# Kernel tuning notes

Hardware: AMD Instinct MI355X
Metric: run time of the kernel (lower is better)

## Reference

```python
import jax, jax.numpy as jnp
import numpy as np
from jax import lax

IN_CH = 512
OUT_CH = 512
KERNEL = 3
STYLE_DIM = 512
BATCH = 8
HW = 64
EPS = 1e-08
LR_MUL = 1.0


def setup_inputs() -> dict:
    key = jax.random.key(0)
    k1, k2, k3, k4 = jax.random.split(key, 4)
    x = jax.random.normal(k1, (BATCH, IN_CH, HW, HW), dtype=jnp.float32)
    style = jax.random.normal(k2, (BATCH, STYLE_DIM), dtype=jnp.float32)
    weight = jax.random.normal(k3, (1, OUT_CH, IN_CH, KERNEL, KERNEL), dtype=jnp.float32)
    mod_weight = jax.random.normal(k4, (IN_CH, STYLE_DIM), dtype=jnp.float32)
    mod_bias = jnp.ones((IN_CH,), dtype=jnp.float32)  # bias_init=1
    return {"x": x, "style": style, "weight": weight,
            "mod_weight": mod_weight, "mod_bias": mod_bias}


def reference(x, style, weight, mod_weight, mod_bias):
    batch, in_ch, h, w_dim = x.shape
    conv_scale = 1.0 / np.sqrt(in_ch * KERNEL * KERNEL)
    lin_scale = 1.0 / np.sqrt(STYLE_DIM) * LR_MUL

    # EqualizedLinear modulation: style -> per-channel scale, shape (B, in_ch)
    s = style @ (mod_weight * lin_scale).T + mod_bias * LR_MUL

    # Modulate: (B, out, in, k, k)
    w = conv_scale * weight * s[:, None, :, None, None]
    # Demodulate
    demod = lax.rsqrt(jnp.sum(w * w, axis=(2, 3, 4)) + EPS)  # (B, out)
    w = w * demod[:, :, None, None, None]

    pad = KERNEL // 2

    def conv_one(xi, wi):
        # xi: (in, H, W), wi: (out, in, k, k)
        return lax.conv_general_dilated(
            xi[None], wi, window_strides=(1, 1),
            padding=[(pad, pad), (pad, pad)],
            dimension_numbers=("NCHW", "OIHW", "NCHW"))[0]

    out = jax.vmap(conv_one)(x, w)  # (B, out, H, W)
    return out
```

## Files before the change

kernel.cpp:

```cpp
#include <hip/hip_runtime.h>
#include <hip/hip_bf16.h>
#include <cstdint>

#define IN_CH 512
#define OUT_CH 512
#define STYLE_DIM 512
#define BATCH 8
#define HW 64

typedef __bf16 bf16x8 __attribute__((ext_vector_type(8)));
typedef float f32x16 __attribute__((ext_vector_type(16)));

__device__ __forceinline__ void gload_lds16(const void* g, void* l) {
  __builtin_amdgcn_global_load_lds(
      (const __attribute__((address_space(1))) unsigned int*)g,
      (__attribute__((address_space(3))) unsigned int*)l,
      16, 0, 0);
}

#define WAITV(N) asm volatile("s_waitcnt vmcnt(" #N ")" ::: "memory")
#define BARRIER() do { asm volatile("" ::: "memory"); __builtin_amdgcn_s_barrier(); \
                       asm volatile("" ::: "memory"); } while (0)

__global__ void k_prepA(const float* __restrict__ style, const float* __restrict__ modw,
                        const float* __restrict__ modb, const float* __restrict__ w,
                        float* __restrict__ s_out, float* __restrict__ wsq,
                        __bf16* __restrict__ wgp) {
  const int tid = threadIdx.x;
  if (blockIdx.x < 128) {
    __shared__ float st[BATCH * STYLE_DIM];
    for (int i = tid; i < BATCH * STYLE_DIM; i += 256) st[i] = style[i];
    __syncthreads();
    const int ic = blockIdx.x * 4 + (tid >> 6);
    const int l = tid & 63;
    const float* mr = modw + (size_t)ic * STYLE_DIM + l * 8;
    float m[8];
    #pragma unroll
    for (int j = 0; j < 8; ++j) m[j] = mr[j];
    float accs[8];
    #pragma unroll
    for (int b = 0; b < 8; ++b) {
      const float* sb = st + b * STYLE_DIM + l * 8;
      float a = 0.f;
      #pragma unroll
      for (int j = 0; j < 8; ++j) a += m[j] * sb[j];
      accs[b] = a;
    }
    #pragma unroll
    for (int off = 32; off; off >>= 1) {
      #pragma unroll
      for (int b = 0; b < 8; ++b) accs[b] += __shfl_down(accs[b], off, 64);
    }
    if (l == 0) {
      #pragma unroll
      for (int b = 0; b < 8; ++b)
        s_out[b * IN_CH + ic] = accs[b] * 0.04419417382415922f + modb[ic];
    }
  } else {
    const int idx = (blockIdx.x - 128) * 256 + tid;
    const int oc = idx >> 9, ic = idx & 511;
    const int octile = oc >> 8, R = oc & 255, j = R >> 1;
    const int chunk = ic >> 6, sslot = (ic >> 3) & 7, e = ic & 7;
    const int p = 2 * ((sslot + j) & 7) + (R & 1);
    const int u = j * 16 + p;
    const float* pw = w + ((size_t)oc * IN_CH + ic) * 9;
    float sum = 0.f;
    #pragma unroll
    for (int t = 0; t < 9; ++t) {
      float v = pw[t];
      sum += v * v;
      wgp[((size_t)((t * 8 + chunk) * 2 + octile) * 2048 + u) * 8 + e] = (__bf16)v;
    }
    wsq[oc * IN_CH + ic] = sum;
  }
}

__global__ void k_prepB(const float* __restrict__ x, const float* __restrict__ s,
                        const float* __restrict__ wsq,
                        __bf16* __restrict__ xgp, float* __restrict__ scale) {
  const int t = threadIdx.x;
  if (blockIdx.x < 512) {
    const int b = blockIdx.x >> 6, y = blockIdx.x & 63;
    const int xcol = t & 63;
    const int g0 = t >> 6;
    const float* sr = s + b * IN_CH;
    const size_t rowbase = ((size_t)(b * 64 + y)) * 8 * 528;
    #pragma unroll
    for (int i = 0; i < 8; ++i) {
      const int g = i * 8 + g0;
      bf16x8 pk;
      #pragma unroll
      for (int e = 0; e < 8; ++e) {
        const int ic = g * 8 + e;
        pk[e] = (__bf16)(x[(((size_t)(b * IN_CH) + ic) * HW + y) * HW + xcol] * sr[ic]);
      }
      const int col = xcol + 1, c = col >> 1;
      const int p = 2 * (((g & 7) + c) & 7) + (col & 1);
      const int u = c * 16 + p;
      *(bf16x8*)(xgp + (rowbase + (size_t)(g >> 3) * 528 + u) * 8) = pk;
    }
    if (t < 128) {
      const int col = (t & 1) * 65, g = t >> 1;
      const int c = col >> 1;
      const int p = 2 * (((g & 7) + c) & 7) + (col & 1);
      const int u = c * 16 + p;
      bf16x8 z = {};
      *(bf16x8*)(xgp + (rowbase + (size_t)(g >> 3) * 528 + u) * 8) = z;
    }
  } else {
    const int oc = (blockIdx.x - 512) * 8 + (t >> 6);
    const int l = t & 63;
    const float* wr = wsq + (size_t)oc * IN_CH + l * 8;
    float w8[8];
    #pragma unroll
    for (int j = 0; j < 8; ++j) w8[j] = wr[j];
    #pragma unroll
    for (int b = 0; b < 8; ++b) {
      const float* sb = s + b * IN_CH + l * 8;
      float acc = 0.f;
      #pragma unroll
      for (int j = 0; j < 8; ++j) { float sv = sb[j]; acc += sv * sv * w8[j]; }
      #pragma unroll
      for (int off = 32; off; off >>= 1) acc += __shfl_down(acc, off, 64);
      if (l == 0)
        scale[b * OUT_CH + oc] =
            rsqrtf(acc * (1.0f / 4608.0f) + 1e-8f) * 0.014731391274719732f;
    }
  }
}

__global__ __launch_bounds__(512, 2) void k_conv(
    const __bf16* __restrict__ Wgp,
    const __bf16* __restrict__ Xgp,
    const float* __restrict__ scale,
    const __bf16* __restrict__ zpg,
    float* __restrict__ out)
{
  __shared__ __attribute__((aligned(16))) __bf16 Xs[3584 * 8];
  __shared__ __attribute__((aligned(16))) __bf16 Wl[3][2048 * 8];

  const int tid = threadIdx.x;
  const int lane = tid & 63;
  const int wid = tid >> 6;
  const int wm = wid >> 2;
  const int wn = wid & 3;
  const int ln31 = lane & 31;
  const int laneK = lane >> 5;

  const int bid0 = blockIdx.x;
  const int bid = (bid0 & 7) * 32 + (bid0 >> 3);
  const int octile = bid & 1;
  const int ptile = (bid >> 1) & 15;
  const int b = bid >> 5;
  const int r0 = ptile * 4;
  const int oc0 = octile * 256;

  auto stage_w = [&](int chunkv, int tapv, int bsel) {
    const __bf16* base = Wgp + (size_t)((tapv * 8 + chunkv) * 2 + octile) * (2048 * 8);
    #pragma unroll
    for (int i = 0; i < 4; ++i) {
      const int u = i * 512 + tid;
      gload_lds16(base + (size_t)u * 8, (void*)((char*)Wl[bsel] + u * 16));
    }
  };
  auto stage_x = [&](int chunkv) {
    #pragma unroll
    for (int i = 0; i < 7; ++i) {
      const unsigned u = i * 512 + tid;
      const unsigned row = u / 528u;
      const unsigned rr = u - row * 528u;
      const int y = r0 - 1 + (int)row;
      const bool ok = (u < 3168u) & (y >= 0) & (y < HW);
      const __bf16* src = ok
          ? Xgp + (((size_t)(b * 64 + y) * 8 + chunkv) * 528 + rr) * 8
          : zpg;
      gload_lds16(src, (void*)((char*)Xs + u * 16));
    }
  };

  stage_x(0);
  stage_w(0, 0, 0);
  stage_w(0, 1, 1);

  int aoff8[4];
  #pragma unroll
  for (int ks = 0; ks < 4; ++ks) aoff8[ks] = ((ln31 + 4 * ks + 2 * laneK) & 15) * 8;
  int bele[3][4];
  #pragma unroll
  for (int dxi = 0; dxi < 3; ++dxi) {
    const int col = ln31 + dxi, c = col >> 1;
    #pragma unroll
    for (int ks = 0; ks < 4; ++ks) {
      const int pos = (col & 1) + 2 * ((2 * ks + laneK + c) & 7);
      bele[dxi][ks] = c * 128 + pos * 8;
    }
  }
  const __bf16* __restrict__ ab0 = Wl[0] + (64 * wm + (ln31 >> 1)) * 128;
  const __bf16* __restrict__ ab1 = Wl[1] + (64 * wm + (ln31 >> 1)) * 128;
  const __bf16* __restrict__ ab2 = Wl[2] + (64 * wm + (ln31 >> 1)) * 128;

  f32x16 acc[4][2] = {};

#define TAPBODY(T) { \
    if ((T) == 8 && c == 7) { WAITV(0); } else { WAITV(4); } \
    BARRIER(); \
    const __bf16* __restrict__ abase = ((T) % 3 == 0) ? ab0 : ((T) % 3 == 1) ? ab1 : ab2; \
    const __bf16* __restrict__ xbase = Xs + (wn + (T) / 3) * (33 * 128); \
    _Pragma("unroll") \
    for (int ks = 0; ks < 4; ++ks) { \
      const int ael = aoff8[ks]; \
      const int bel = bele[(T) % 3][ks]; \
      bf16x8 av[4], bv[2]; \
      _Pragma("unroll") \
      for (int mf = 0; mf < 4; ++mf) av[mf] = *(const bf16x8*)(abase + mf * 2048 + ael); \
      bv[0] = *(const bf16x8*)(xbase + bel); \
      bv[1] = *(const bf16x8*)(xbase + 2048 + bel); \
      _Pragma("unroll") \
      for (int mf = 0; mf < 4; ++mf) { \
        acc[mf][0] = __builtin_amdgcn_mfma_f32_32x32x16_bf16(av[mf], bv[0], acc[mf][0], 0, 0, 0); \
        acc[mf][1] = __builtin_amdgcn_mfma_f32_32x32x16_bf16(av[mf], bv[1], acc[mf][1], 0, 0, 0); \
      } \
    } \
    if ((T) == 8) { \
      if (c < 7) { BARRIER(); stage_x(c + 1); stage_w(c + 1, 1, 1); } \
    } else if ((T) <= 6) { \
      stage_w(c, (T) + 2, ((T) + 2) % 3); \
    } else {  \
      if (c < 7) stage_w(c + 1, 0, 0); \
    } \
  }

  #pragma unroll 1
  for (int c = 0; c < 8; ++c) {
    TAPBODY(0) TAPBODY(1) TAPBODY(2)
    TAPBODY(3) TAPBODY(4) TAPBODY(5)
    TAPBODY(6) TAPBODY(7) TAPBODY(8)
  }

  const int y = r0 + wn;
  #pragma unroll
  for (int mf = 0; mf < 4; ++mf) {
    #pragma unroll
    for (int reg = 0; reg < 16; ++reg) {
      const int rowid = (reg & 3) + 8 * (reg >> 2) + 4 * laneK;
      const int oc = oc0 + 128 * wm + 32 * mf + rowid;
      const float sc = scale[b * OUT_CH + oc];
      float* op = out + (((size_t)(b * OUT_CH + oc) * HW + y) * HW) + ln31;
      op[0] = acc[mf][0][reg] * sc;
      op[32] = acc[mf][1][reg] * sc;
    }
  }
}

extern "C" void kernel_launch(void* const* d_in, const int* in_sizes, int n_in,
                              void* d_out, int out_size, void* d_ws, size_t ws_size,
                              hipStream_t stream) {
  const float* x      = (const float*)d_in[0];
  const float* style  = (const float*)d_in[1];
  const float* weight = (const float*)d_in[2];
  const float* modw   = (const float*)d_in[3];
  const float* modb   = (const float*)d_in[4];
  float* out = (float*)d_out;

  char* ws = (char*)d_ws;
  float*  s_buf = (float*)(ws + 0);
  float*  scale = (float*)(ws + 16384);
  __bf16* zpg   = (__bf16*)(ws + 32768);
  float*  wsq   = (float*)(ws + 49152);
  __bf16* wgp   = (__bf16*)(ws + 49152 + 1048576);
  __bf16* xgp   = (__bf16*)(ws + 49152 + 1048576 + 9 * 8 * 2 * 2048 * 8 * 2);

  hipMemsetAsync(zpg, 0, 16384, stream);
  k_prepA<<<1152, 256, 0, stream>>>(style, modw, modb, weight, s_buf, wsq, wgp);
  k_prepB<<<576, 512, 0, stream>>>(x, s_buf, wsq, xgp, scale);
  k_conv<<<256, 512, 0, stream>>>(wgp, xgp, scale, zpg, out);
}
```

Before: 161.3 us.

## Rebalance prep kernels, fold memset, stagger k-order and prefetch next-tap B fragments

The prep stage is reorganised. A small style kernel now computes the modulation and zeroes the padding buffer, which removes the separate memset launch. A combined prep kernel packs x, packs the weights and computes the demod scale directly from the weights, dropping the wsq intermediate buffer. In the conv kernel each wave starts its k-slice loop at a different offset to spread LDS bank access, and the first B fragments for the next tap are loaded early so their latency overlaps the MFMAs. The cost is extra register pressure and recomputing the weight squares per output-channel block.

```diff
diff --git a/kernel.cpp b/kernel.cpp
--- a/kernel.cpp
+++ b/kernel.cpp
@@ -22,98 +22,101 @@
 #define BARRIER() do { asm volatile("" ::: "memory"); __builtin_amdgcn_s_barrier(); \
                        asm volatile("" ::: "memory"); } while (0)
 
-__global__ void k_prepA(const float* __restrict__ style, const float* __restrict__ modw,
-                        const float* __restrict__ modb, const float* __restrict__ w,
-                        float* __restrict__ s_out, float* __restrict__ wsq,
-                        __bf16* __restrict__ wgp) {
+__global__ void k_style(const float* __restrict__ style, const float* __restrict__ modw,
+                        const float* __restrict__ modb, float* __restrict__ s_out,
+                        float* __restrict__ zpg) {
   const int tid = threadIdx.x;
-  if (blockIdx.x < 128) {
-    __shared__ float st[BATCH * STYLE_DIM];
-    for (int i = tid; i < BATCH * STYLE_DIM; i += 256) st[i] = style[i];
-    __syncthreads();
-    const int ic = blockIdx.x * 4 + (tid >> 6);
-    const int l = tid & 63;
-    const float* mr = modw + (size_t)ic * STYLE_DIM + l * 8;
-    float m[8];
-    #pragma unroll
-    for (int j = 0; j < 8; ++j) m[j] = mr[j];
-    float accs[8];
-    #pragma unroll
-    for (int b = 0; b < 8; ++b) {
-      const float* sb = st + b * STYLE_DIM + l * 8;
-      float a = 0.f;
-      #pragma unroll
-      for (int j = 0; j < 8; ++j) a += m[j] * sb[j];
-      accs[b] = a;
-    }
-    #pragma unroll
-    for (int off = 32; off; off >>= 1) {
-      #pragma unroll
-      for (int b = 0; b < 8; ++b) accs[b] += __shfl_down(accs[b], off, 64);
-    }
-    if (l == 0) {
-      #pragma unroll
-      for (int b = 0; b < 8; ++b)
-        s_out[b * IN_CH + ic] = accs[b] * 0.04419417382415922f + modb[ic];
-    }
-  } else {
-    const int idx = (blockIdx.x - 128) * 256 + tid;
+  if (blockIdx.x == 128) {
+    float4 z = {0.f, 0.f, 0.f, 0.f};
+    #pragma unroll
+    for (int k = 0; k < 4; ++k) ((float4*)zpg)[tid * 4 + k] = z;
+    return;
+  }
+  __shared__ float st[BATCH * STYLE_DIM];
+  for (int i = tid; i < BATCH * STYLE_DIM; i += 256) st[i] = style[i];
+  __syncthreads();
+  const int ic = blockIdx.x * 4 + (tid >> 6);
+  const int l = tid & 63;
+  const float* mr = modw + (size_t)ic * STYLE_DIM + l * 8;
+  float m[8];
+  #pragma unroll
+  for (int j = 0; j < 8; ++j) m[j] = mr[j];
+  float accs[8];
+  #pragma unroll
+  for (int b = 0; b < 8; ++b) {
+    const float* sb = st + b * STYLE_DIM + l * 8;
+    float a = 0.f;
+    #pragma unroll
+    for (int j = 0; j < 8; ++j) a += m[j] * sb[j];
+    accs[b] = a;
+  }
+  #pragma unroll
+  for (int off = 32; off; off >>= 1) {
+    #pragma unroll
+    for (int b = 0; b < 8; ++b) accs[b] += __shfl_down(accs[b], off, 64);
+  }
+  if (l == 0) {
+    #pragma unroll
+    for (int b = 0; b < 8; ++b)
+      s_out[b * IN_CH + ic] = accs[b] * 0.04419417382415922f + modb[ic];
+  }
+}
+
+__global__ void k_prep(const float* __restrict__ x, const float* __restrict__ s,
+                       const float* __restrict__ w,
+                       __bf16* __restrict__ xgp, __bf16* __restrict__ wgp,
+                       float* __restrict__ scale) {
+  const int t = threadIdx.x;
+  const int bid = blockIdx.x;
+  if (bid < 512) {
+    const int b = bid >> 6, y = bid & 63;
+    const int xcol = t & 63;
+    const int g0 = t >> 6;
+    const float* sr = s + b * IN_CH;
+    const size_t rowbase = ((size_t)(b * 64 + y)) * 8 * 528;
+    #pragma unroll
+    for (int i = 0; i < 8; ++i) {
+      const int g = i * 8 + g0;
+      bf16x8 pk;
+      #pragma unroll
+      for (int e = 0; e < 8; ++e) {
+        const int ic = g * 8 + e;
+        pk[e] = (__bf16)(x[(((size_t)(b * IN_CH) + ic) * HW + y) * HW + xcol] * sr[ic]);
+      }
+      const int col = xcol + 1, c = col >> 1;
+      const int p = 2 * (((g & 7) + c) & 7) + (col & 1);
+      *(bf16x8*)(xgp + (rowbase + (size_t)(g >> 3) * 528 + c * 16 + p) * 8) = pk;
+    }
+    if (t < 128) {
+      const int col = (t & 1) * 65, g = t >> 1;
+      const int c = col >> 1;
+      const int p = 2 * (((g & 7) + c) & 7) + (col & 1);
+      bf16x8 z = {};
+      *(bf16x8*)(xgp + (rowbase + (size_t)(g >> 3) * 528 + c * 16 + p) * 8) = z;
+    }
+  } else if (bid < 1024) {
+    const int idx = (bid - 512) * 512 + t;
     const int oc = idx >> 9, ic = idx & 511;
     const int octile = oc >> 8, R = oc & 255, j = R >> 1;
     const int chunk = ic >> 6, sslot = (ic >> 3) & 7, e = ic & 7;
     const int p = 2 * ((sslot + j) & 7) + (R & 1);
     const int u = j * 16 + p;
     const float* pw = w + ((size_t)oc * IN_CH + ic) * 9;
-    float sum = 0.f;
-    #pragma unroll
-    for (int t = 0; t < 9; ++t) {
-      float v = pw[t];
-      sum += v * v;
-      wgp[((size_t)((t * 8 + chunk) * 2 + octile) * 2048 + u) * 8 + e] = (__bf16)v;
-    }
-    wsq[oc * IN_CH + ic] = sum;
-  }
-}
-
-__global__ void k_prepB(const float* __restrict__ x, const float* __restrict__ s,
-                        const float* __restrict__ wsq,
-                        __bf16* __restrict__ xgp, float* __restrict__ scale) {
-  const int t = threadIdx.x;
-  if (blockIdx.x < 512) {
-    const int b = blockIdx.x >> 6, y = blockIdx.x & 63;
-    const int xcol = t & 63;
-    const int g0 = t >> 6;
-    const float* sr = s + b * IN_CH;
-    const size_t rowbase = ((size_t)(b * 64 + y)) * 8 * 528;
-    #pragma unroll
-    for (int i = 0; i < 8; ++i) {
-      const int g = i * 8 + g0;
-      bf16x8 pk;
-      #pragma unroll
-      for (int e = 0; e < 8; ++e) {
-        const int ic = g * 8 + e;
-        pk[e] = (__bf16)(x[(((size_t)(b * IN_CH) + ic) * HW + y) * HW + xcol] * sr[ic]);
-      }
-      const int col = xcol + 1, c = col >> 1;
-      const int p = 2 * (((g & 7) + c) & 7) + (col & 1);
-      const int u = c * 16 + p;
-      *(bf16x8*)(xgp + (rowbase + (size_t)(g >> 3) * 528 + u) * 8) = pk;
-    }
-    if (t < 128) {
-      const int col = (t & 1) * 65, g = t >> 1;
-      const int c = col >> 1;
-      const int p = 2 * (((g & 7) + c) & 7) + (col & 1);
-      const int u = c * 16 + p;
-      bf16x8 z = {};
-      *(bf16x8*)(xgp + (rowbase + (size_t)(g >> 3) * 528 + u) * 8) = z;
-    }
+    #pragma unroll
+    for (int tp = 0; tp < 9; ++tp)
+      wgp[((size_t)((tp * 8 + chunk) * 2 + octile) * 2048 + u) * 8 + e] = (__bf16)pw[tp];
   } else {
-    const int oc = (blockIdx.x - 512) * 8 + (t >> 6);
+    const int oc = (bid - 1024) * 8 + (t >> 6);
     const int l = t & 63;
-    const float* wr = wsq + (size_t)oc * IN_CH + l * 8;
     float w8[8];
     #pragma unroll
-    for (int j = 0; j < 8; ++j) w8[j] = wr[j];
+    for (int j = 0; j < 8; ++j) {
+      const float* pw = w + ((size_t)oc * IN_CH + l * 8 + j) * 9;
+      float sum = 0.f;
+      #pragma unroll
+      for (int tp = 0; tp < 9; ++tp) { float v = pw[tp]; sum += v * v; }
+      w8[j] = sum;
+    }
     #pragma unroll
     for (int b = 0; b < 8; ++b) {
       const float* sb = s + b * IN_CH + l * 8;
@@ -146,6 +149,7 @@
   const int wn = wid & 3;
   const int ln31 = lane & 31;
   const int laneK = lane >> 5;
+  const int kord = wid & 3;
 
   const int bid0 = blockIdx.x;
   const int bid = (bid0 & 7) * 32 + (bid0 >> 3);
@@ -182,17 +186,18 @@
   stage_w(0, 0, 0);
   stage_w(0, 1, 1);
 
-  int aoff8[4];
-  #pragma unroll
-  for (int ks = 0; ks < 4; ++ks) aoff8[ks] = ((ln31 + 4 * ks + 2 * laneK) & 15) * 8;
-  int bele[3][4];
+  int aoffR[4];
+  #pragma unroll
+  for (int i = 0; i < 4; ++i)
+    aoffR[i] = ((ln31 + 4 * (kord + i) + 2 * laneK) & 15) * 8;
+  int beleR[3][4];
   #pragma unroll
   for (int dxi = 0; dxi < 3; ++dxi) {
     const int col = ln31 + dxi, c = col >> 1;
     #pragma unroll
-    for (int ks = 0; ks < 4; ++ks) {
-      const int pos = (col & 1) + 2 * ((2 * ks + laneK + c) & 7);
-      bele[dxi][ks] = c * 128 + pos * 8;
+    for (int i = 0; i < 4; ++i) {
+      const int pos = (col & 1) + 2 * ((2 * (kord + i) + laneK + c) & 7);
+      beleR[dxi][i] = c * 128 + pos * 8;
     }
   }
   const __bf16* __restrict__ ab0 = Wl[0] + (64 * wm + (ln31 >> 1)) * 128;
@@ -200,6 +205,7 @@
   const __bf16* __restrict__ ab2 = Wl[2] + (64 * wm + (ln31 >> 1)) * 128;
 
   f32x16 acc[4][2] = {};
+  bf16x8 bvp0, bvp1;
 
 #define TAPBODY(T) { \
     if ((T) == 8 && c == 7) { WAITV(0); } else { WAITV(4); } \
@@ -207,19 +213,26 @@
     const __bf16* __restrict__ abase = ((T) % 3 == 0) ? ab0 : ((T) % 3 == 1) ? ab1 : ab2; \
     const __bf16* __restrict__ xbase = Xs + (wn + (T) / 3) * (33 * 128); \
     _Pragma("unroll") \
-    for (int ks = 0; ks < 4; ++ks) { \
-      const int ael = aoff8[ks]; \
-      const int bel = bele[(T) % 3][ks]; \
+    for (int i = 0; i < 4; ++i) { \
+      const int ael = aoffR[i]; \
+      const int bel = beleR[(T) % 3][i]; \
       bf16x8 av[4], bv[2]; \
       _Pragma("unroll") \
       for (int mf = 0; mf < 4; ++mf) av[mf] = *(const bf16x8*)(abase + mf * 2048 + ael); \
-      bv[0] = *(const bf16x8*)(xbase + bel); \
-      bv[1] = *(const bf16x8*)(xbase + 2048 + bel); \
+      if ((T) > 0 && i == 0) { bv[0] = bvp0; bv[1] = bvp1; } \
+      else { bv[0] = *(const bf16x8*)(xbase + bel); \
+             bv[1] = *(const bf16x8*)(xbase + 2048 + bel); } \
       _Pragma("unroll") \
       for (int mf = 0; mf < 4; ++mf) { \
         acc[mf][0] = __builtin_amdgcn_mfma_f32_32x32x16_bf16(av[mf], bv[0], acc[mf][0], 0, 0, 0); \
         acc[mf][1] = __builtin_amdgcn_mfma_f32_32x32x16_bf16(av[mf], bv[1], acc[mf][1], 0, 0, 0); \
       } \
+    } \
+    if ((T) < 8) {    \
+      const __bf16* __restrict__ xn = Xs + (wn + ((T) + 1) / 3) * (33 * 128); \
+      const int beln = beleR[((T) + 1) % 3][0]; \
+      bvp0 = *(const bf16x8*)(xn + beln); \
+      bvp1 = *(const bf16x8*)(xn + 2048 + beln); \
     } \
     if ((T) == 8) { \
       if (c < 7) { BARRIER(); stage_x(c + 1); stage_w(c + 1, 1, 1); } \
@@ -266,12 +279,10 @@
   float*  s_buf = (float*)(ws + 0);
   float*  scale = (float*)(ws + 16384);
   __bf16* zpg   = (__bf16*)(ws + 32768);
-  float*  wsq   = (float*)(ws + 49152);
-  __bf16* wgp   = (__bf16*)(ws + 49152 + 1048576);
-  __bf16* xgp   = (__bf16*)(ws + 49152 + 1048576 + 9 * 8 * 2 * 2048 * 8 * 2);
-
-  hipMemsetAsync(zpg, 0, 16384, stream);
-  k_prepA<<<1152, 256, 0, stream>>>(style, modw, modb, weight, s_buf, wsq, wgp);
-  k_prepB<<<576, 512, 0, stream>>>(x, s_buf, wsq, xgp, scale);
+  __bf16* wgp   = (__bf16*)(ws + 49152);
+  __bf16* xgp   = (__bf16*)(ws + 49152 + 9 * 8 * 2 * 2048 * 8 * 2);
+
+  k_style<<<129, 256, 0, stream>>>(style, modw, modb, s_buf, (float*)zpg);
+  k_prep<<<1088, 512, 0, stream>>>(x, s_buf, weight, xgp, wgp, scale);
   k_conv<<<256, 512, 0, stream>>>(wgp, xgp, scale, zpg, out);
 }
```

Result: no change. 160.5 us (-0.5%).
